# Performance work log

Measured on AMD Instinct MI355X. Metric: run time of the kernel, lower is better.

## Reference

```python
import jax, jax.numpy as jnp
import numpy as np

HIDDEN = 450
DEPTH = 6
ATOM_FDIM = 35          # len(ELEM_LIST)+6+5+1
BOND_FDIM = 5
MAX_NB = 15
N_ATOMS = 20000
N_BONDS = 40000
N_MESS = 16000          # tree messages (row 0 is the zero padding slot)
N_MOLS = 1000


def _linear_init(key, out_dim, in_dim):
    s = 1.0 / np.sqrt(in_dim)
    return jax.random.uniform(key, (out_dim, in_dim), jnp.float32, -s, s)


def setup_inputs() -> dict:
    key = jax.random.key(0)
    ks = jax.random.split(key, 9)
    total_msg = N_MESS + N_BONDS
    fatoms = jax.random.normal(ks[0], (N_ATOMS, ATOM_FDIM), jnp.float32)
    fbonds = jax.random.normal(ks[1], (N_BONDS, ATOM_FDIM + BOND_FDIM), jnp.float32)
    agraph = jax.random.randint(ks[2], (N_ATOMS, MAX_NB), 0, total_msg, jnp.int32)
    bgraph = jax.random.randint(ks[3], (N_BONDS, MAX_NB), 0, total_msg, jnp.int32)
    tree_message = jax.random.normal(ks[4], (N_MESS, HIDDEN), jnp.float32)
    tree_message = tree_message.at[0].set(0.0)  # index 0 = padding message
    # uniform scope: N_MOLS molecules of N_ATOMS//N_MOLS atoms each
    mol_ids = jnp.repeat(jnp.arange(N_MOLS, dtype=jnp.int32), N_ATOMS // N_MOLS)
    W_i = _linear_init(ks[5], HIDDEN, ATOM_FDIM + BOND_FDIM)
    W_h = _linear_init(ks[6], HIDDEN, HIDDEN)
    W_o = _linear_init(ks[7], HIDDEN, ATOM_FDIM + HIDDEN)
    s = 1.0 / np.sqrt(ATOM_FDIM + HIDDEN)
    b_o = jax.random.uniform(ks[8], (HIDDEN,), jnp.float32, -s, s)
    return {"fatoms": fatoms, "fbonds": fbonds, "agraph": agraph, "bgraph": bgraph,
            "mol_ids": mol_ids, "n_mols": N_MOLS, "tree_message": tree_message,
            "W_i": W_i, "W_h": W_h, "W_o": W_o, "b_o": b_o}


def reference(fatoms, fbonds, agraph, bgraph, mol_ids, n_mols, tree_message,
              W_i, W_h, W_o, b_o):
    binput = fbonds @ W_i.T                       # [B, H]
    graph_message = jax.nn.relu(binput)
    for _ in range(DEPTH - 1):                    # static depth loop
        message = jnp.concatenate([tree_message, graph_message], axis=0)  # [M+B, H]
        nei_message = message[bgraph].sum(axis=1)  # gather [B, MAX_NB, H] -> [B, H]
        graph_message = jax.nn.relu(binput + nei_message @ W_h.T)
    message = jnp.concatenate([tree_message, graph_message], axis=0)
    nei_message = message[agraph].sum(axis=1)      # [A, H]
    ainput = jnp.concatenate([fatoms, nei_message], axis=1)  # [A, ATOM_FDIM+H]
    atom_hiddens = jax.nn.relu(ainput @ W_o.T + b_o)          # [A, H]
    # mean over each molecule's atoms (scope)
    sums = jax.ops.segment_sum(atom_hiddens, mol_ids, num_segments=n_mols)
    counts = jax.ops.segment_sum(jnp.ones((atom_hiddens.shape[0], 1), atom_hiddens.dtype),
                                 mol_ids, num_segments=n_mols)
    return sums / counts
```

## Files before the change

kernel.cpp:

```cpp
#include <hip/hip_runtime.h>

#define HIDDEN 450
#define MAX_NB 15
#define N_ATOMS 20000
#define N_BONDS 40000
#define N_MESS  16000
#define N_MOLS  1000
#define KPAD    512
#define MSTRIDE 456
#define FSTRIDE 64
#define BM      64

typedef unsigned int uint;
typedef unsigned short ushort;
typedef __bf16 bf16x8 __attribute__((ext_vector_type(8)));
typedef float  f32x4  __attribute__((ext_vector_type(4)));

__device__ __forceinline__ ushort f2bf(float f) {
    uint u = __builtin_bit_cast(uint, f);
    u += 0x7fffu + ((u >> 16) & 1u);
    return (ushort)(u >> 16);
}
__device__ __forceinline__ float bfhi(uint w) {
    return __builtin_bit_cast(float, w & 0xffff0000u);
}
__device__ __forceinline__ float bflo(uint w) {
    return __builtin_bit_cast(float, w << 16);
}


__global__ __launch_bounds__(256) void pack_tree(const float* __restrict__ tree,
                                                 ushort* __restrict__ tbuf) {
    const int r = blockIdx.x, t = threadIdx.x;
    if (t < 228) {
        uint p = 0;
        if (t < 225) {
            const float2 v = *(const float2*)&tree[(size_t)r * HIDDEN + 2 * t];
            p = (uint)f2bf(v.x) | ((uint)f2bf(v.y) << 16);
        }
        ((uint*)(tbuf + (size_t)r * MSTRIDE))[t] = p;
    }
}

__global__ __launch_bounds__(256) void pack_bonds(const float* __restrict__ fbonds,
                                                  ushort* __restrict__ Abuf) {
    const int r = blockIdx.x * 4 + (threadIdx.x >> 6);
    const int t = threadIdx.x & 63;
    if (r >= N_BONDS) return;
    Abuf[(size_t)r * FSTRIDE + t] = (t < 40) ? f2bf(fbonds[(size_t)r * 40 + t])
                                             : (ushort)0;
}

__global__ __launch_bounds__(256) void pack_atoms(const float* __restrict__ fatoms,
                                                  ushort* __restrict__ Aout) {
    const int r = blockIdx.x * 4 + (threadIdx.x >> 6);
    const int t = threadIdx.x & 63;
    if (r >= N_ATOMS) return;
    Aout[(size_t)r * FSTRIDE + t] = (t < 35) ? f2bf(fatoms[(size_t)r * 35 + t])
                                             : (ushort)0;
}

__global__ __launch_bounds__(256) void pack_w(const float* __restrict__ W_i,
                                              const float* __restrict__ W_h,
                                              const float* __restrict__ W_o,
                                              ushort* __restrict__ Wcat,
                                              ushort* __restrict__ Wocat) {
    const int n = blockIdx.x;
    for (int c = threadIdx.x; c < KPAD; c += 256) {
        float v = 0.0f, vo = 0.0f;
        if (n < HIDDEN) {
            if (c < 40)       v = W_i[(size_t)n * 40 + c];
            else if (c < 490) v = W_h[(size_t)n * HIDDEN + (c - 40)];
            if (c < 35)       vo = W_o[(size_t)n * 485 + c];
            else if (c >= 40 && c < 490) vo = W_o[(size_t)n * 485 + 35 + (c - 40)];
        }
        Wcat [(size_t)n * KPAD + c] = f2bf(v);
        Wocat[(size_t)n * KPAD + c] = f2bf(vo);
    }
}

__global__ __launch_bounds__(256) void precompute_base(const int* __restrict__ g,
                                                       const ushort* __restrict__ tbuf,
                                                       ushort* __restrict__ base,
                                                       int nrows) {
    const int r_raw = blockIdx.x * 4 + (threadIdx.x >> 6);
    const int lane = threadIdx.x & 63;
    if (r_raw >= nrows) return;
    const int r = __builtin_amdgcn_readfirstlane(r_raw);
    const int* gr = g + (size_t)r * MAX_NB;
    const ushort* p[MAX_NB];
#pragma unroll
    for (int j = 0; j < MAX_NB; ++j) {
        const int idx = gr[j];
        p[j] = tbuf + (size_t)((idx < N_MESS) ? idx : 0) * MSTRIDE;
    }
    if (lane >= 57) return;
    const int off = lane * 8;
    uint4 w[MAX_NB];
#pragma unroll
    for (int j = 0; j < MAX_NB; ++j) w[j] = *(const uint4*)(p[j] + off);
    __builtin_amdgcn_sched_barrier(0);
    float acc[8] = {};
#pragma unroll
    for (int j = 0; j < MAX_NB; ++j) {
        acc[0] += bflo(w[j].x); acc[1] += bfhi(w[j].x);
        acc[2] += bflo(w[j].y); acc[3] += bfhi(w[j].y);
        acc[4] += bflo(w[j].z); acc[5] += bfhi(w[j].z);
        acc[6] += bflo(w[j].w); acc[7] += bfhi(w[j].w);
    }
    uint4 o;
    o.x = (uint)f2bf(acc[0]) | ((uint)f2bf(acc[1]) << 16);
    o.y = (uint)f2bf(acc[2]) | ((uint)f2bf(acc[3]) << 16);
    o.z = (uint)f2bf(acc[4]) | ((uint)f2bf(acc[5]) << 16);
    o.w = (uint)f2bf(acc[6]) | ((uint)f2bf(acc[7]) << 16);
    *(uint4*)(base + (size_t)r * MSTRIDE + off) = o;
}

template <int KT, int AST>
__global__ __launch_bounds__(256, 2) void mfma_gemm0(
    const ushort* __restrict__ A, int M,
    const ushort* __restrict__ W,
    ushort* __restrict__ gout, int mtiles) {
    __shared__ ushort At[64 * KT * 32];
    const int tid = threadIdx.x;
    const int id  = blockIdx.x;
    const int b     = id & 7;
    const int n_blk = (id >> 3) & 1;
    const int m_blk = (id >> 4) * 8 + b;
    if (m_blk >= mtiles) return;
    const int m0 = m_blk * 64, n0 = n_blk * 256;
    const int CPR = KT * 4;

    {
        const int srow = tid >> 2;
        const int c0   = tid & 3;
        const ushort* gsrc = A + (size_t)min(m0 + srow, M - 1) * AST;
        ushort* lrow = At + srow * (KT * 32);
#pragma unroll
        for (int c = c0; c < CPR; c += 4) {
            const uint4 v = *(const uint4*)(gsrc + c * 8);
            *(uint4*)&lrow[(c ^ (srow & 7)) * 8] = v;
        }
    }
    __syncthreads();

    const int lane = tid & 63;
    const int wave = tid >> 6;
    const int wn = wave * 64;
    const int lr = lane & 15;
    const int lk = lane >> 4;

    size_t woff[4];
#pragma unroll
    for (int s = 0; s < 4; ++s)
        woff[s] = (size_t)(n0 + wn + s * 16 + lr) * KPAD + lk * 8;

    f32x4 acc[4][4];
#pragma unroll
    for (int i = 0; i < 4; ++i)
#pragma unroll
        for (int j = 0; j < 4; ++j) acc[i][j] = (f32x4){0.f, 0.f, 0.f, 0.f};

    bf16x8 wa[4], wb[4], afa[4];
#pragma unroll
    for (int s = 0; s < 4; ++s) wa[s] = *(const bf16x8*)&W[woff[s]];
#pragma unroll
    for (int s = 0; s < 4; ++s)
        wb[s] = (KT > 1) ? *(const bf16x8*)&W[woff[s] + 32] : wa[s];
#pragma unroll
    for (int mt = 0; mt < 4; ++mt) {
        const int row = mt * 16 + lr;
        afa[mt] = *(const bf16x8*)&At[(row * CPR + (lk ^ (row & 7))) * 8];
    }

#pragma unroll
    for (int i = 0; i < KT; ++i) {
        bf16x8 wc[4], afb[4];
        if (i + 2 < KT) {
#pragma unroll
            for (int s = 0; s < 4; ++s)
                wc[s] = *(const bf16x8*)&W[woff[s] + (size_t)(i + 2) * 32];
        }
        if (i + 1 < KT) {
#pragma unroll
            for (int mt = 0; mt < 4; ++mt) {
                const int row = mt * 16 + lr;
                const int chunk = (((i + 1) * 4 + lk)) ^ (row & 7);
                afb[mt] = *(const bf16x8*)&At[(row * CPR + chunk) * 8];
            }
        }
#pragma unroll
        for (int mt = 0; mt < 4; ++mt)
#pragma unroll
            for (int nt = 0; nt < 4; ++nt)
                acc[mt][nt] = __builtin_amdgcn_mfma_f32_16x16x32_bf16(
                    afa[mt], wa[nt], acc[mt][nt], 0, 0, 0);
        if (i + 1 < KT) {
#pragma unroll
            for (int s = 0; s < 4; ++s) wa[s] = wb[s];
#pragma unroll
            for (int mt = 0; mt < 4; ++mt) afa[mt] = afb[mt];
        }
        if (i + 2 < KT) {
#pragma unroll
            for (int s = 0; s < 4; ++s) wb[s] = wc[s];
        }
    }

    const int col_l = lane & 15;
    const int rbase = (lane >> 4) * 4;
#pragma unroll
    for (int mt = 0; mt < 4; ++mt) {
        const int mbase = m0 + mt * 16 + rbase;
#pragma unroll
        for (int nt = 0; nt < 4; ++nt) {
            const int n = n0 + wn + nt * 16 + col_l;
#pragma unroll
            for (int reg = 0; reg < 4; ++reg) {
                const int m = mbase + reg;
                if (m >= M) continue;
                if (n < HIDDEN)
                    gout[(size_t)m * MSTRIDE + n] = f2bf(fmaxf(acc[mt][nt][reg], 0.0f));
                else if (n < MSTRIDE)
                    gout[(size_t)m * MSTRIDE + n] = 0;
            }
        }
    }
}

template <int MODE>
__global__ __launch_bounds__(512, 4) void fused_gg(
    const int* __restrict__ g,
    const ushort* __restrict__ base,
    const ushort* __restrict__ gin,
    const ushort* __restrict__ zrow,
    const ushort* __restrict__ feat,
    const ushort* __restrict__ W,
    const float* __restrict__ bias, const int* __restrict__ mol_ids,
    ushort* __restrict__ gout, float* __restrict__ aout, int M) {
    __shared__ ushort At[BM * KPAD];
    const int tid  = threadIdx.x;
    const int lane = tid & 63;
    const int wave = tid >> 6;
    const int m0 = blockIdx.x * BM;

#pragma unroll 1
    for (int rr = 0; rr < 8; ++rr) {
        const int r = (wave << 3) | rr;
        const int m = __builtin_amdgcn_readfirstlane(min(m0 + r, M - 1));
        const int sw = r & 7;
        ushort* lrow = At + r * KPAD;
        const int* gr = g + (size_t)m * MAX_NB;
        const ushort* p[MAX_NB];
#pragma unroll
        for (int j = 0; j < MAX_NB; ++j) {
            const int row = gr[j] - N_MESS;
            p[j] = (row >= 0) ? gin + (size_t)row * MSTRIDE : zrow;
        }
        if (lane < 57) {
            const int off = lane * 8;
            const uint4 b = *(const uint4*)(base + (size_t)m * MSTRIDE + off);
            uint4 w[MAX_NB];
#pragma unroll
            for (int j = 0; j < MAX_NB; ++j) w[j] = *(const uint4*)(p[j] + off);
            __builtin_amdgcn_sched_barrier(0);
            float acc[8];
            acc[0] = bflo(b.x); acc[1] = bfhi(b.x);
            acc[2] = bflo(b.y); acc[3] = bfhi(b.y);
            acc[4] = bflo(b.z); acc[5] = bfhi(b.z);
            acc[6] = bflo(b.w); acc[7] = bfhi(b.w);
#pragma unroll
            for (int j = 0; j < MAX_NB; ++j) {
                acc[0] += bflo(w[j].x); acc[1] += bfhi(w[j].x);
                acc[2] += bflo(w[j].y); acc[3] += bfhi(w[j].y);
                acc[4] += bflo(w[j].z); acc[5] += bfhi(w[j].z);
                acc[6] += bflo(w[j].w); acc[7] += bfhi(w[j].w);
            }
            uint4 o;
            o.x = (uint)f2bf(acc[0]) | ((uint)f2bf(acc[1]) << 16);
            o.y = (uint)f2bf(acc[2]) | ((uint)f2bf(acc[3]) << 16);
            o.z = (uint)f2bf(acc[4]) | ((uint)f2bf(acc[5]) << 16);
            o.w = (uint)f2bf(acc[6]) | ((uint)f2bf(acc[7]) << 16);
            *(uint4*)&lrow[((5 + lane) ^ sw) * 8] = o;
        } else {
            const int c = (lane < 62) ? (lane - 57) : lane;
            uint4 v = (uint4){0u, 0u, 0u, 0u};
            if (lane < 62)
                v = *(const uint4*)(feat + (size_t)m * FSTRIDE + (lane - 57) * 8);
            *(uint4*)&lrow[(c ^ sw) * 8] = v;
        }
    }
    __syncthreads();

    const int wn = wave * 64;
    const int lr = lane & 15;
    const int lk = lane >> 4;

    size_t woff[4];
#pragma unroll
    for (int s = 0; s < 4; ++s)
        woff[s] = (size_t)(wn + s * 16 + lr) * KPAD + lk * 8;

    f32x4 acc[4][4];
#pragma unroll
    for (int i = 0; i < 4; ++i)
#pragma unroll
        for (int j = 0; j < 4; ++j) acc[i][j] = (f32x4){0.f, 0.f, 0.f, 0.f};

    bf16x8 wa[4], wb[4], afa[4];
#pragma unroll
    for (int s = 0; s < 4; ++s) wa[s] = *(const bf16x8*)&W[woff[s]];
#pragma unroll
    for (int s = 0; s < 4; ++s) wb[s] = *(const bf16x8*)&W[woff[s] + 32];
#pragma unroll
    for (int mt = 0; mt < 4; ++mt) {
        const int row = mt * 16 + lr;
        afa[mt] = *(const bf16x8*)&At[(row * 64 + (lk ^ (row & 7))) * 8];
    }

#pragma unroll
    for (int i = 0; i < 16; ++i) {
        bf16x8 wc[4], afb[4];
        if (i + 2 < 16) {
#pragma unroll
            for (int s = 0; s < 4; ++s)
                wc[s] = *(const bf16x8*)&W[woff[s] + (size_t)(i + 2) * 32];
        }
        if (i + 1 < 16) {
#pragma unroll
            for (int mt = 0; mt < 4; ++mt) {
                const int row = mt * 16 + lr;
                const int chunk = (((i + 1) * 4 + lk)) ^ (row & 7);
                afb[mt] = *(const bf16x8*)&At[(row * 64 + chunk) * 8];
            }
        }
#pragma unroll
        for (int mt = 0; mt < 4; ++mt)
#pragma unroll
            for (int nt = 0; nt < 4; ++nt)
                acc[mt][nt] = __builtin_amdgcn_mfma_f32_16x16x32_bf16(
                    afa[mt], wa[nt], acc[mt][nt], 0, 0, 0);
        if (i + 1 < 16) {
#pragma unroll
            for (int s = 0; s < 4; ++s) wa[s] = wb[s];
#pragma unroll
            for (int mt = 0; mt < 4; ++mt) afa[mt] = afb[mt];
        }
        if (i + 2 < 16) {
#pragma unroll
            for (int s = 0; s < 4; ++s) wb[s] = wc[s];
        }
    }

    const int col_l = lane & 15;
    const int rbase = (lane >> 4) * 4;
#pragma unroll
    for (int mt = 0; mt < 4; ++mt) {
        const int mbase = m0 + mt * 16 + rbase;
        int mol[4];
        if (MODE == 1) {
#pragma unroll
            for (int reg = 0; reg < 4; ++reg)
                mol[reg] = mol_ids[min(mbase + reg, M - 1)];
        }
#pragma unroll
        for (int nt = 0; nt < 4; ++nt) {
            const int n = wn + nt * 16 + col_l;
            if (MODE == 0) {
#pragma unroll
                for (int reg = 0; reg < 4; ++reg) {
                    const int m = mbase + reg;
                    if (m >= M) continue;
                    if (n < HIDDEN)
                        gout[(size_t)m * MSTRIDE + n] = f2bf(fmaxf(acc[mt][nt][reg], 0.0f));
                    else if (n < MSTRIDE)
                        gout[(size_t)m * MSTRIDE + n] = 0;
                }
            } else {
                if (n >= HIDDEN) continue;
                const float bsum = bias[n];
                float run = 0.0f;
                int cur = mol[0];
#pragma unroll
                for (int reg = 0; reg < 4; ++reg) {
                    const float v = (mbase + reg < M)
                        ? fmaxf(acc[mt][nt][reg] + bsum, 0.0f) : 0.0f;
                    if (mol[reg] != cur) {
                        atomicAdd(&aout[(size_t)cur * HIDDEN + n], run);
                        cur = mol[reg];
                        run = 0.0f;
                    }
                    run += v;
                }
                atomicAdd(&aout[(size_t)cur * HIDDEN + n], run);
            }
        }
    }
}

__global__ __launch_bounds__(256) void count_atoms(const int* __restrict__ mol_ids,
                                                   float* __restrict__ counts) {
    const int a = blockIdx.x * 256 + threadIdx.x;
    if (a < N_ATOMS) atomicAdd(&counts[mol_ids[a]], 1.0f);
}
__global__ __launch_bounds__(256) void div_counts(float* __restrict__ out,
                                                  const float* __restrict__ counts) {
    const int i = blockIdx.x * 256 + threadIdx.x;
    if (i < N_MOLS * HIDDEN) out[i] = out[i] / counts[i / HIDDEN];
}

extern "C" void kernel_launch(void* const* d_in, const int* in_sizes, int n_in,
                              void* d_out, int out_size, void* d_ws, size_t ws_size,
                              hipStream_t stream) {
    const float* fatoms  = (const float*)d_in[0];
    const float* fbonds  = (const float*)d_in[1];
    const int*   agraph  = (const int*)d_in[2];
    const int*   bgraph  = (const int*)d_in[3];
    const int*   mol_ids = (const int*)d_in[4];
    const float* tree    = (const float*)d_in[6];
    const float* W_i     = (const float*)d_in[7];
    const float* W_h     = (const float*)d_in[8];
    const float* W_o     = (const float*)d_in[9];
    const float* b_o     = (const float*)d_in[10];
    float* out = (float*)d_out;

    ushort* zrow   = (ushort*)d_ws;
    ushort* Abuf   = zrow   + 512;
    ushort* Aout   = Abuf   + (size_t)N_BONDS * FSTRIDE;
    ushort* gmsgA  = Aout   + (size_t)N_ATOMS * FSTRIDE;
    ushort* gmsgB  = gmsgA  + (size_t)N_BONDS * MSTRIDE;
    ushort* tbuf   = gmsgB  + (size_t)N_BONDS * MSTRIDE;
    ushort* Wcat   = tbuf   + (size_t)N_MESS  * MSTRIDE;
    ushort* Wocat  = Wcat   + (size_t)KPAD * KPAD;
    ushort* base_b = Wocat  + (size_t)KPAD * KPAD;
    ushort* base_a = base_b + (size_t)N_BONDS * MSTRIDE;
    float*  counts = (float*)(base_a + (size_t)N_ATOMS * MSTRIDE);

    (void)hipMemsetAsync(d_out, 0, (size_t)N_MOLS * HIDDEN * sizeof(float), stream);
    (void)hipMemsetAsync(counts, 0, N_MOLS * sizeof(float), stream);
    (void)hipMemsetAsync(zrow, 0, 512 * sizeof(ushort), stream);

    const dim3 blk(256);
    pack_tree <<<N_MESS, blk, 0, stream>>>(tree, tbuf);
    pack_bonds<<<(N_BONDS + 3) / 4, blk, 0, stream>>>(fbonds, Abuf);
    pack_atoms<<<(N_ATOMS + 3) / 4, blk, 0, stream>>>(fatoms, Aout);
    pack_w    <<<KPAD, blk, 0, stream>>>(W_i, W_h, W_o, Wcat, Wocat);
    precompute_base<<<(N_BONDS + 3) / 4, blk, 0, stream>>>(bgraph, tbuf, base_b, N_BONDS);
    precompute_base<<<(N_ATOMS + 3) / 4, blk, 0, stream>>>(agraph, tbuf, base_a, N_ATOMS);

    const int mtB = (N_BONDS + 63) / 64;
    const int mtA = (N_ATOMS + 63) / 64;
    const dim3 gB0(((mtB + 7) / 8) * 16);

    mfma_gemm0<2, FSTRIDE><<<gB0, blk, 0, stream>>>(Abuf, N_BONDS, Wcat, gmsgA, mtB);

    ushort* cur = gmsgA;
    ushort* nxt = gmsgB;
    const dim3 blk2(512);
    for (int it = 0; it < 5; ++it) {
        fused_gg<0><<<mtB, blk2, 0, stream>>>(bgraph, base_b, cur, zrow, Abuf, Wcat,
                                              nullptr, nullptr, nxt, nullptr, N_BONDS);
        ushort* t = cur; cur = nxt; nxt = t;
    }
    fused_gg<1><<<mtA, blk2, 0, stream>>>(agraph, base_a, cur, zrow, Aout, Wocat,
                                          b_o, mol_ids, nullptr, out, N_ATOMS);

    count_atoms<<<(N_ATOMS + 255) / 256, blk, 0, stream>>>(mol_ids, counts);
    div_counts <<<(N_MOLS * HIDDEN + 255) / 256, blk, 0, stream>>>(out, counts);
}
```

Measured before the change: 835.9 us.

## Double-buffer gather/GEMM tiles in fused kernel and drop atom base precompute

The fused gather+GEMM kernel now processes two 32-row tiles per block with two LDS buffers, staging the second tile's neighbour gather while the first tile's MFMA loop runs. The atom-side precompute of tree-message sums is removed; the final atom kernel gathers tree messages directly from the packed tree buffer instead. This aims to overlap memory-bound gathers with matrix work and skip one full precompute pass, at the cost of smaller M tiles (less W reuse per tile) and more gathers in the final kernel.

New measurement: 1.050 ms. 1.26x slower.

```diff
diff --git a/kernel.cpp b/kernel.cpp
--- a/kernel.cpp
+++ b/kernel.cpp
@@ -9,7 +9,7 @@
 #define KPAD    512
 #define MSTRIDE 456
 #define FSTRIDE 64
-#define BM      64
+#define BM      32
 
 typedef unsigned int uint;
 typedef unsigned short ushort;
@@ -228,173 +228,201 @@
     }
 }
 
-template <int MODE>
+template <int MODE, bool HASBASE>
 __global__ __launch_bounds__(512, 4) void fused_gg(
     const int* __restrict__ g,
     const ushort* __restrict__ base,
     const ushort* __restrict__ gin,
     const ushort* __restrict__ zrow,
+    const ushort* __restrict__ tmsg,
     const ushort* __restrict__ feat,
     const ushort* __restrict__ W,
     const float* __restrict__ bias, const int* __restrict__ mol_ids,
-    ushort* __restrict__ gout, float* __restrict__ aout, int M) {
-    __shared__ ushort At[BM * KPAD];
+    ushort* __restrict__ gout, float* __restrict__ aout, int M, int mtiles) {
+    __shared__ ushort At[2][BM * KPAD];
     const int tid  = threadIdx.x;
     const int lane = tid & 63;
     const int wave = tid >> 6;
-    const int m0 = blockIdx.x * BM;
-
-#pragma unroll 1
-    for (int rr = 0; rr < 8; ++rr) {
-        const int r = (wave << 3) | rr;
-        const int m = __builtin_amdgcn_readfirstlane(min(m0 + r, M - 1));
-        const int sw = r & 7;
-        ushort* lrow = At + r * KPAD;
-        const int* gr = g + (size_t)m * MAX_NB;
-        const ushort* p[MAX_NB];
-#pragma unroll
-        for (int j = 0; j < MAX_NB; ++j) {
-            const int row = gr[j] - N_MESS;
-            p[j] = (row >= 0) ? gin + (size_t)row * MSTRIDE : zrow;
-        }
-        if (lane < 57) {
-            const int off = lane * 8;
-            const uint4 b = *(const uint4*)(base + (size_t)m * MSTRIDE + off);
-            uint4 w[MAX_NB];
-#pragma unroll
-            for (int j = 0; j < MAX_NB; ++j) w[j] = *(const uint4*)(p[j] + off);
-            __builtin_amdgcn_sched_barrier(0);
-            float acc[8];
-            acc[0] = bflo(b.x); acc[1] = bfhi(b.x);
-            acc[2] = bflo(b.y); acc[3] = bfhi(b.y);
-            acc[4] = bflo(b.z); acc[5] = bfhi(b.z);
-            acc[6] = bflo(b.w); acc[7] = bfhi(b.w);
-#pragma unroll
-            for (int j = 0; j < MAX_NB; ++j) {
-                acc[0] += bflo(w[j].x); acc[1] += bfhi(w[j].x);
-                acc[2] += bflo(w[j].y); acc[3] += bfhi(w[j].y);
-                acc[4] += bflo(w[j].z); acc[5] += bfhi(w[j].z);
-                acc[6] += bflo(w[j].w); acc[7] += bfhi(w[j].w);
-            }
-            uint4 o;
-            o.x = (uint)f2bf(acc[0]) | ((uint)f2bf(acc[1]) << 16);
-            o.y = (uint)f2bf(acc[2]) | ((uint)f2bf(acc[3]) << 16);
-            o.z = (uint)f2bf(acc[4]) | ((uint)f2bf(acc[5]) << 16);
-            o.w = (uint)f2bf(acc[6]) | ((uint)f2bf(acc[7]) << 16);
-            *(uint4*)&lrow[((5 + lane) ^ sw) * 8] = o;
-        } else {
-            const int c = (lane < 62) ? (lane - 57) : lane;
-            uint4 v = (uint4){0u, 0u, 0u, 0u};
-            if (lane < 62)
-                v = *(const uint4*)(feat + (size_t)m * FSTRIDE + (lane - 57) * 8);
-            *(uint4*)&lrow[(c ^ sw) * 8] = v;
-        }
-    }
-    __syncthreads();
-
-    const int wn = wave * 64;
     const int lr = lane & 15;
     const int lk = lane >> 4;
+    const int wn = wave * 64;
+    const int t0 = blockIdx.x * 2;
 
     size_t woff[4];
 #pragma unroll
     for (int s = 0; s < 4; ++s)
         woff[s] = (size_t)(wn + s * 16 + lr) * KPAD + lk * 8;
 
-    f32x4 acc[4][4];
-#pragma unroll
-    for (int i = 0; i < 4; ++i)
-#pragma unroll
-        for (int j = 0; j < 4; ++j) acc[i][j] = (f32x4){0.f, 0.f, 0.f, 0.f};
-
-    bf16x8 wa[4], wb[4], afa[4];
-#pragma unroll
-    for (int s = 0; s < 4; ++s) wa[s] = *(const bf16x8*)&W[woff[s]];
-#pragma unroll
-    for (int s = 0; s < 4; ++s) wb[s] = *(const bf16x8*)&W[woff[s] + 32];
-#pragma unroll
-    for (int mt = 0; mt < 4; ++mt) {
-        const int row = mt * 16 + lr;
-        afa[mt] = *(const bf16x8*)&At[(row * 64 + (lk ^ (row & 7))) * 8];
-    }
-
-#pragma unroll
-    for (int i = 0; i < 16; ++i) {
-        bf16x8 wc[4], afb[4];
-        if (i + 2 < 16) {
-#pragma unroll
-            for (int s = 0; s < 4; ++s)
-                wc[s] = *(const bf16x8*)&W[woff[s] + (size_t)(i + 2) * 32];
-        }
-        if (i + 1 < 16) {
-#pragma unroll
-            for (int mt = 0; mt < 4; ++mt) {
-                const int row = mt * 16 + lr;
-                const int chunk = (((i + 1) * 4 + lk)) ^ (row & 7);
-                afb[mt] = *(const bf16x8*)&At[(row * 64 + chunk) * 8];
-            }
-        }
-#pragma unroll
-        for (int mt = 0; mt < 4; ++mt)
-#pragma unroll
-            for (int nt = 0; nt < 4; ++nt)
-                acc[mt][nt] = __builtin_amdgcn_mfma_f32_16x16x32_bf16(
-                    afa[mt], wa[nt], acc[mt][nt], 0, 0, 0);
-        if (i + 1 < 16) {
-#pragma unroll
-            for (int s = 0; s < 4; ++s) wa[s] = wb[s];
-#pragma unroll
-            for (int mt = 0; mt < 4; ++mt) afa[mt] = afb[mt];
-        }
-        if (i + 2 < 16) {
-#pragma unroll
-            for (int s = 0; s < 4; ++s) wb[s] = wc[s];
-        }
-    }
-
-    const int col_l = lane & 15;
-    const int rbase = (lane >> 4) * 4;
-#pragma unroll
-    for (int mt = 0; mt < 4; ++mt) {
-        const int mbase = m0 + mt * 16 + rbase;
-        int mol[4];
-        if (MODE == 1) {
-#pragma unroll
-            for (int reg = 0; reg < 4; ++reg)
-                mol[reg] = mol_ids[min(mbase + reg, M - 1)];
-        }
-#pragma unroll
-        for (int nt = 0; nt < 4; ++nt) {
-            const int n = wn + nt * 16 + col_l;
-            if (MODE == 0) {
-#pragma unroll
-                for (int reg = 0; reg < 4; ++reg) {
-                    const int m = mbase + reg;
-                    if (m >= M) continue;
-                    if (n < HIDDEN)
-                        gout[(size_t)m * MSTRIDE + n] = f2bf(fmaxf(acc[mt][nt][reg], 0.0f));
-                    else if (n < MSTRIDE)
-                        gout[(size_t)m * MSTRIDE + n] = 0;
+    auto STAGE = [&](int tile, ushort* buf) {
+#pragma unroll 1
+        for (int rr = 0; rr < 4; ++rr) {
+            const int r = (wave << 2) | rr;
+            const int m = __builtin_amdgcn_readfirstlane(min(tile * BM + r, M - 1));
+            const int sw = r & 7;
+            ushort* lrow = buf + r * KPAD;
+            const int* gr = g + (size_t)m * MAX_NB;
+            const ushort* p[MAX_NB];
+#pragma unroll
+            for (int j = 0; j < MAX_NB; ++j) {
+                const int idx = gr[j];
+                const int row = idx - N_MESS;
+                if (HASBASE) p[j] = (row >= 0) ? gin + (size_t)row * MSTRIDE : zrow;
+                else p[j] = (row >= 0) ? gin + (size_t)row * MSTRIDE
+                                       : tmsg + (size_t)idx * MSTRIDE;
+            }
+            if (lane < 57) {
+                const int off = lane * 8;
+                float acc[8];
+                uint4 w[MAX_NB];
+                if (HASBASE) {
+                    const uint4 b = *(const uint4*)(base + (size_t)m * MSTRIDE + off);
+#pragma unroll
+                    for (int j = 0; j < MAX_NB; ++j)
+                        w[j] = *(const uint4*)(p[j] + off);
+                    __builtin_amdgcn_sched_barrier(0);
+                    acc[0] = bflo(b.x); acc[1] = bfhi(b.x);
+                    acc[2] = bflo(b.y); acc[3] = bfhi(b.y);
+                    acc[4] = bflo(b.z); acc[5] = bfhi(b.z);
+                    acc[6] = bflo(b.w); acc[7] = bfhi(b.w);
+                } else {
+#pragma unroll
+                    for (int j = 0; j < MAX_NB; ++j)
+                        w[j] = *(const uint4*)(p[j] + off);
+                    __builtin_amdgcn_sched_barrier(0);
+#pragma unroll
+                    for (int k = 0; k < 8; ++k) acc[k] = 0.0f;
                 }
+#pragma unroll
+                for (int j = 0; j < MAX_NB; ++j) {
+                    acc[0] += bflo(w[j].x); acc[1] += bfhi(w[j].x);
+                    acc[2] += bflo(w[j].y); acc[3] += bfhi(w[j].y);
+                    acc[4] += bflo(w[j].z); acc[5] += bfhi(w[j].z);
+                    acc[6] += bflo(w[j].w); acc[7] += bfhi(w[j].w);
+                }
+                uint4 o;
+                o.x = (uint)f2bf(acc[0]) | ((uint)f2bf(acc[1]) << 16);
+                o.y = (uint)f2bf(acc[2]) | ((uint)f2bf(acc[3]) << 16);
+                o.z = (uint)f2bf(acc[4]) | ((uint)f2bf(acc[5]) << 16);
+                o.w = (uint)f2bf(acc[6]) | ((uint)f2bf(acc[7]) << 16);
+                *(uint4*)&lrow[((5 + lane) ^ sw) * 8] = o;
             } else {
-                if (n >= HIDDEN) continue;
-                const float bsum = bias[n];
-                float run = 0.0f;
-                int cur = mol[0];
-#pragma unroll
-                for (int reg = 0; reg < 4; ++reg) {
-                    const float v = (mbase + reg < M)
-                        ? fmaxf(acc[mt][nt][reg] + bsum, 0.0f) : 0.0f;
-                    if (mol[reg] != cur) {
-                        atomicAdd(&aout[(size_t)cur * HIDDEN + n], run);
-                        cur = mol[reg];
-                        run = 0.0f;
+                const int c = (lane < 62) ? (lane - 57) : lane;
+                uint4 v = (uint4){0u, 0u, 0u, 0u};
+                if (lane < 62)
+                    v = *(const uint4*)(feat + (size_t)m * FSTRIDE + (lane - 57) * 8);
+                *(uint4*)&lrow[(c ^ sw) * 8] = v;
+            }
+        }
+    };
+
+    auto COMPUTE = [&](int tile, const ushort* buf) {
+        const int m0 = tile * BM;
+        f32x4 acc[2][4];
+#pragma unroll
+        for (int i = 0; i < 2; ++i)
+#pragma unroll
+            for (int j = 0; j < 4; ++j) acc[i][j] = (f32x4){0.f, 0.f, 0.f, 0.f};
+
+        bf16x8 wa[4], wb[4], afa[2];
+#pragma unroll
+        for (int s = 0; s < 4; ++s) wa[s] = *(const bf16x8*)&W[woff[s]];
+#pragma unroll
+        for (int s = 0; s < 4; ++s) wb[s] = *(const bf16x8*)&W[woff[s] + 32];
+#pragma unroll
+        for (int mt = 0; mt < 2; ++mt) {
+            const int row = mt * 16 + lr;
+            afa[mt] = *(const bf16x8*)&buf[(row * 64 + (lk ^ (row & 7))) * 8];
+        }
+
+#pragma unroll
+        for (int i = 0; i < 16; ++i) {
+            bf16x8 wc[4], afb[2];
+            if (i + 2 < 16) {
+#pragma unroll
+                for (int s = 0; s < 4; ++s)
+                    wc[s] = *(const bf16x8*)&W[woff[s] + (size_t)(i + 2) * 32];
+            }
+            if (i + 1 < 16) {
+#pragma unroll
+                for (int mt = 0; mt < 2; ++mt) {
+                    const int row = mt * 16 + lr;
+                    const int chunk = (((i + 1) * 4 + lk)) ^ (row & 7);
+                    afb[mt] = *(const bf16x8*)&buf[(row * 64 + chunk) * 8];
+                }
+            }
+#pragma unroll
+            for (int mt = 0; mt < 2; ++mt)
+#pragma unroll
+                for (int nt = 0; nt < 4; ++nt)
+                    acc[mt][nt] = __builtin_amdgcn_mfma_f32_16x16x32_bf16(
+                        afa[mt], wa[nt], acc[mt][nt], 0, 0, 0);
+            if (i + 1 < 16) {
+#pragma unroll
+                for (int s = 0; s < 4; ++s) wa[s] = wb[s];
+#pragma unroll
+                for (int mt = 0; mt < 2; ++mt) afa[mt] = afb[mt];
+            }
+            if (i + 2 < 16) {
+#pragma unroll
+                for (int s = 0; s < 4; ++s) wb[s] = wc[s];
+            }
+        }
+
+        const int col_l = lane & 15;
+        const int rbase = (lane >> 4) * 4;
+#pragma unroll
+        for (int mt = 0; mt < 2; ++mt) {
+            const int mbase = m0 + mt * 16 + rbase;
+            int mol[4];
+            if (MODE == 1) {
+#pragma unroll
+                for (int reg = 0; reg < 4; ++reg)
+                    mol[reg] = mol_ids[min(mbase + reg, M - 1)];
+            }
+#pragma unroll
+            for (int nt = 0; nt < 4; ++nt) {
+                const int n = wn + nt * 16 + col_l;
+                if (MODE == 0) {
+#pragma unroll
+                    for (int reg = 0; reg < 4; ++reg) {
+                        const int m = mbase + reg;
+                        if (m >= M) continue;
+                        if (n < HIDDEN)
+                            gout[(size_t)m * MSTRIDE + n] =
+                                f2bf(fmaxf(acc[mt][nt][reg], 0.0f));
+                        else if (n < MSTRIDE)
+                            gout[(size_t)m * MSTRIDE + n] = 0;
                     }
-                    run += v;
+                } else {
+                    if (n >= HIDDEN) continue;
+                    const float bsum = bias[n];
+                    float run = 0.0f;
+                    int cur = mol[0];
+#pragma unroll
+                    for (int reg = 0; reg < 4; ++reg) {
+                        const float v = (mbase + reg < M)
+                            ? fmaxf(acc[mt][nt][reg] + bsum, 0.0f) : 0.0f;
+                        if (mol[reg] != cur) {
+                            atomicAdd(&aout[(size_t)cur * HIDDEN + n], run);
+                            cur = mol[reg];
+                            run = 0.0f;
+                        }
+                        run += v;
+                    }
+                    atomicAdd(&aout[(size_t)cur * HIDDEN + n], run);
                 }
-                atomicAdd(&aout[(size_t)cur * HIDDEN + n], run);
-            }
-        }
+            }
+        }
+    };
+
+    STAGE(t0, At[0]);
+    __syncthreads();
+    const bool has2 = (t0 + 1 < mtiles);
+    if (has2) STAGE(t0 + 1, At[1]);
+    COMPUTE(t0, At[0]);
+    if (has2) {
+        __syncthreads();
+        COMPUTE(t0 + 1, At[1]);
     }
 }
 
@@ -433,8 +461,7 @@
     ushort* Wcat   = tbuf   + (size_t)N_MESS  * MSTRIDE;
     ushort* Wocat  = Wcat   + (size_t)KPAD * KPAD;
     ushort* base_b = Wocat  + (size_t)KPAD * KPAD;
-    ushort* base_a = base_b + (size_t)N_BONDS * MSTRIDE;
-    float*  counts = (float*)(base_a + (size_t)N_ATOMS * MSTRIDE);
+    float*  counts = (float*)(base_b + (size_t)N_BONDS * MSTRIDE);
 
     (void)hipMemsetAsync(d_out, 0, (size_t)N_MOLS * HIDDEN * sizeof(float), stream);
     (void)hipMemsetAsync(counts, 0, N_MOLS * sizeof(float), stream);
@@ -446,24 +473,28 @@
     pack_atoms<<<(N_ATOMS + 3) / 4, blk, 0, stream>>>(fatoms, Aout);
     pack_w    <<<KPAD, blk, 0, stream>>>(W_i, W_h, W_o, Wcat, Wocat);
     precompute_base<<<(N_BONDS + 3) / 4, blk, 0, stream>>>(bgraph, tbuf, base_b, N_BONDS);
-    precompute_base<<<(N_ATOMS + 3) / 4, blk, 0, stream>>>(agraph, tbuf, base_a, N_ATOMS);
-
-    const int mtB = (N_BONDS + 63) / 64;
-    const int mtA = (N_ATOMS + 63) / 64;
-    const dim3 gB0(((mtB + 7) / 8) * 16);
-
-    mfma_gemm0<2, FSTRIDE><<<gB0, blk, 0, stream>>>(Abuf, N_BONDS, Wcat, gmsgA, mtB);
-
+
+    const int mt64 = (N_BONDS + 63) / 64;
+    const dim3 gB0(((mt64 + 7) / 8) * 16);
+
+    mfma_gemm0<2, FSTRIDE><<<gB0, blk, 0, stream>>>(Abuf, N_BONDS, Wcat, gmsgA, mt64);
+
+    const int mtB = (N_BONDS + BM - 1) / BM;
+    const int mtA = (N_ATOMS + BM - 1) / BM;
     ushort* cur = gmsgA;
     ushort* nxt = gmsgB;
     const dim3 blk2(512);
+    const dim3 gB((mtB + 1) / 2);
+    const dim3 gA((mtA + 1) / 2);
     for (int it = 0; it < 5; ++it) {
-        fused_gg<0><<<mtB, blk2, 0, stream>>>(bgraph, base_b, cur, zrow, Abuf, Wcat,
-                                              nullptr, nullptr, nxt, nullptr, N_BONDS);
+        fused_gg<0, true><<<gB, blk2, 0, stream>>>(bgraph, base_b, cur, zrow, tbuf,
+                                                   Abuf, Wcat, nullptr, nullptr,
+                                                   nxt, nullptr, N_BONDS, mtB);
         ushort* t = cur; cur = nxt; nxt = t;
     }
-    fused_gg<1><<<mtA, blk2, 0, stream>>>(agraph, base_a, cur, zrow, Aout, Wocat,
-                                          b_o, mol_ids, nullptr, out, N_ATOMS);
+    fused_gg<1, false><<<gA, blk2, 0, stream>>>(agraph, nullptr, cur, zrow, tbuf,
+                                                Aout, Wocat, b_o, mol_ids,
+                                                nullptr, out, N_ATOMS, mtA);
 
     count_atoms<<<(N_ATOMS + 255) / 256, blk, 0, stream>>>(mol_ids, counts);
     div_counts <<<(N_MOLS * HIDDEN + 255) / 256, blk, 0, stream>>>(out, counts);
```

## Shrink fused gather-GEMM tile to 16 rows with multi-tile blocks and unified message buffer

Applied to the files above, without the earlier changes.

The fused gather+GEMM kernel now works on 16-row tiles instead of 64, and each block loops over several tiles (5 per block for bonds, 3 for atoms) with fixed grid sizes. The workspace is laid out so tree messages and both graph-message buffers sit contiguously and are indexed through one base pointer plus an offset. This removes the zero-row buffer and the separate atom base precompute, since the final atom pass gathers tree messages directly. Each wave now amortises its weight-fragment loads over 4x fewer rows, which raises weight traffic from L2 and adds a second barrier per tile. In exchange it gets finer-grained work and one less precompute kernel.

Result: slower. 2.060 ms (+146.5%).

```diff
diff --git a/kernel.cpp b/kernel.cpp
--- a/kernel.cpp
+++ b/kernel.cpp
@@ -9,7 +9,7 @@
 #define KPAD    512
 #define MSTRIDE 456
 #define FSTRIDE 64
-#define BM      64
+#define BM      16
 
 typedef unsigned int uint;
 typedef unsigned short ushort;
@@ -232,136 +232,137 @@
 __global__ __launch_bounds__(512, 4) void fused_gg(
     const int* __restrict__ g,
     const ushort* __restrict__ base,
-    const ushort* __restrict__ gin,
-    const ushort* __restrict__ zrow,
+    const ushort* __restrict__ msg,
+    int dynoff,
     const ushort* __restrict__ feat,
     const ushort* __restrict__ W,
     const float* __restrict__ bias, const int* __restrict__ mol_ids,
-    ushort* __restrict__ gout, float* __restrict__ aout, int M) {
+    ushort* __restrict__ gout, float* __restrict__ aout,
+    int mtiles, int tpb) {
     __shared__ ushort At[BM * KPAD];
     const int tid  = threadIdx.x;
     const int lane = tid & 63;
     const int wave = tid >> 6;
-    const int m0 = blockIdx.x * BM;
-
-#pragma unroll 1
-    for (int rr = 0; rr < 8; ++rr) {
-        const int r = (wave << 3) | rr;
-        const int m = __builtin_amdgcn_readfirstlane(min(m0 + r, M - 1));
-        const int sw = r & 7;
-        ushort* lrow = At + r * KPAD;
-        const int* gr = g + (size_t)m * MAX_NB;
-        const ushort* p[MAX_NB];
-#pragma unroll
-        for (int j = 0; j < MAX_NB; ++j) {
-            const int row = gr[j] - N_MESS;
-            p[j] = (row >= 0) ? gin + (size_t)row * MSTRIDE : zrow;
-        }
-        if (lane < 57) {
-            const int off = lane * 8;
-            const uint4 b = *(const uint4*)(base + (size_t)m * MSTRIDE + off);
-            uint4 w[MAX_NB];
-#pragma unroll
-            for (int j = 0; j < MAX_NB; ++j) w[j] = *(const uint4*)(p[j] + off);
-            __builtin_amdgcn_sched_barrier(0);
-            float acc[8];
-            acc[0] = bflo(b.x); acc[1] = bfhi(b.x);
-            acc[2] = bflo(b.y); acc[3] = bfhi(b.y);
-            acc[4] = bflo(b.z); acc[5] = bfhi(b.z);
-            acc[6] = bflo(b.w); acc[7] = bfhi(b.w);
-#pragma unroll
-            for (int j = 0; j < MAX_NB; ++j) {
-                acc[0] += bflo(w[j].x); acc[1] += bfhi(w[j].x);
-                acc[2] += bflo(w[j].y); acc[3] += bfhi(w[j].y);
-                acc[4] += bflo(w[j].z); acc[5] += bfhi(w[j].z);
-                acc[6] += bflo(w[j].w); acc[7] += bfhi(w[j].w);
-            }
-            uint4 o;
-            o.x = (uint)f2bf(acc[0]) | ((uint)f2bf(acc[1]) << 16);
-            o.y = (uint)f2bf(acc[2]) | ((uint)f2bf(acc[3]) << 16);
-            o.z = (uint)f2bf(acc[4]) | ((uint)f2bf(acc[5]) << 16);
-            o.w = (uint)f2bf(acc[6]) | ((uint)f2bf(acc[7]) << 16);
-            *(uint4*)&lrow[((5 + lane) ^ sw) * 8] = o;
-        } else {
-            const int c = (lane < 62) ? (lane - 57) : lane;
-            uint4 v = (uint4){0u, 0u, 0u, 0u};
-            if (lane < 62)
-                v = *(const uint4*)(feat + (size_t)m * FSTRIDE + (lane - 57) * 8);
-            *(uint4*)&lrow[(c ^ sw) * 8] = v;
-        }
-    }
-    __syncthreads();
-
-    const int wn = wave * 64;
     const int lr = lane & 15;
     const int lk = lane >> 4;
+    const int wn = wave * 64;
 
     size_t woff[4];
 #pragma unroll
     for (int s = 0; s < 4; ++s)
         woff[s] = (size_t)(wn + s * 16 + lr) * KPAD + lk * 8;
 
-    f32x4 acc[4][4];
-#pragma unroll
-    for (int i = 0; i < 4; ++i)
-#pragma unroll
-        for (int j = 0; j < 4; ++j) acc[i][j] = (f32x4){0.f, 0.f, 0.f, 0.f};
-
-    bf16x8 wa[4], wb[4], afa[4];
-#pragma unroll
-    for (int s = 0; s < 4; ++s) wa[s] = *(const bf16x8*)&W[woff[s]];
-#pragma unroll
-    for (int s = 0; s < 4; ++s) wb[s] = *(const bf16x8*)&W[woff[s] + 32];
-#pragma unroll
-    for (int mt = 0; mt < 4; ++mt) {
-        const int row = mt * 16 + lr;
-        afa[mt] = *(const bf16x8*)&At[(row * 64 + (lk ^ (row & 7))) * 8];
-    }
-
-#pragma unroll
-    for (int i = 0; i < 16; ++i) {
-        bf16x8 wc[4], afb[4];
-        if (i + 2 < 16) {
-#pragma unroll
-            for (int s = 0; s < 4; ++s)
-                wc[s] = *(const bf16x8*)&W[woff[s] + (size_t)(i + 2) * 32];
-        }
-        if (i + 1 < 16) {
-#pragma unroll
-            for (int mt = 0; mt < 4; ++mt) {
-                const int row = mt * 16 + lr;
-                const int chunk = (((i + 1) * 4 + lk)) ^ (row & 7);
-                afb[mt] = *(const bf16x8*)&At[(row * 64 + chunk) * 8];
-            }
-        }
-#pragma unroll
-        for (int mt = 0; mt < 4; ++mt)
+    const int tbeg = blockIdx.x * tpb;
+    const int tend = min(tbeg + tpb, mtiles);
+
+    for (int tile = tbeg; tile < tend; ++tile) {
+#pragma unroll 1
+        for (int rr = 0; rr < 2; ++rr) {
+            const int r = wave * 2 + rr;
+            const int m = __builtin_amdgcn_readfirstlane(tile * BM + r);
+            const int sw = r & 7;
+            ushort* lrow = At + r * KPAD;
+            const int* gr = g + (size_t)m * MAX_NB;
+            const ushort* p[MAX_NB];
+#pragma unroll
+            for (int j = 0; j < MAX_NB; ++j) {
+                const int idx = gr[j];
+                int mrow;
+                if (MODE == 0)
+                    mrow = (idx >= N_MESS) ? (idx - N_MESS + dynoff) : 0;
+                else
+                    mrow = (idx >= N_MESS) ? (idx - N_MESS + dynoff) : idx;
+                p[j] = msg + (size_t)mrow * MSTRIDE;
+            }
+            if (lane < 57) {
+                const int off = lane * 8;
+                uint4 w[MAX_NB];
+                float acc[8];
+                if (MODE == 0) {
+                    const uint4 b = *(const uint4*)(base + (size_t)m * MSTRIDE + off);
+#pragma unroll
+                    for (int j = 0; j < MAX_NB; ++j)
+                        w[j] = *(const uint4*)(p[j] + off);
+                    __builtin_amdgcn_sched_barrier(0);
+                    acc[0] = bflo(b.x); acc[1] = bfhi(b.x);
+                    acc[2] = bflo(b.y); acc[3] = bfhi(b.y);
+                    acc[4] = bflo(b.z); acc[5] = bfhi(b.z);
+                    acc[6] = bflo(b.w); acc[7] = bfhi(b.w);
+                } else {
+#pragma unroll
+                    for (int j = 0; j < MAX_NB; ++j)
+                        w[j] = *(const uint4*)(p[j] + off);
+                    __builtin_amdgcn_sched_barrier(0);
+#pragma unroll
+                    for (int k = 0; k < 8; ++k) acc[k] = 0.0f;
+                }
+#pragma unroll
+                for (int j = 0; j < MAX_NB; ++j) {
+                    acc[0] += bflo(w[j].x); acc[1] += bfhi(w[j].x);
+                    acc[2] += bflo(w[j].y); acc[3] += bfhi(w[j].y);
+                    acc[4] += bflo(w[j].z); acc[5] += bfhi(w[j].z);
+                    acc[6] += bflo(w[j].w); acc[7] += bfhi(w[j].w);
+                }
+                uint4 o;
+                o.x = (uint)f2bf(acc[0]) | ((uint)f2bf(acc[1]) << 16);
+                o.y = (uint)f2bf(acc[2]) | ((uint)f2bf(acc[3]) << 16);
+                o.z = (uint)f2bf(acc[4]) | ((uint)f2bf(acc[5]) << 16);
+                o.w = (uint)f2bf(acc[6]) | ((uint)f2bf(acc[7]) << 16);
+                *(uint4*)&lrow[((5 + lane) ^ sw) * 8] = o;
+            } else {
+                const int c = (lane < 62) ? (lane - 57) : lane;
+                uint4 v = (uint4){0u, 0u, 0u, 0u};
+                if (lane < 62)
+                    v = *(const uint4*)(feat + (size_t)m * FSTRIDE + (lane - 57) * 8);
+                *(uint4*)&lrow[(c ^ sw) * 8] = v;
+            }
+        }
+        __syncthreads();
+
+        f32x4 acc[4];
+#pragma unroll
+        for (int j = 0; j < 4; ++j) acc[j] = (f32x4){0.f, 0.f, 0.f, 0.f};
+
+        bf16x8 wa[4], wb[4];
+#pragma unroll
+        for (int s = 0; s < 4; ++s) wa[s] = *(const bf16x8*)&W[woff[s]];
+#pragma unroll
+        for (int s = 0; s < 4; ++s) wb[s] = *(const bf16x8*)&W[woff[s] + 32];
+        bf16x8 afa = *(const bf16x8*)&At[(lr * 64 + (lk ^ (lr & 7))) * 8];
+
+#pragma unroll
+        for (int i = 0; i < 16; ++i) {
+            bf16x8 wc[4], afb;
+            if (i + 2 < 16) {
+#pragma unroll
+                for (int s = 0; s < 4; ++s)
+                    wc[s] = *(const bf16x8*)&W[woff[s] + (size_t)(i + 2) * 32];
+            }
+            if (i + 1 < 16) {
+                const int chunk = (((i + 1) * 4 + lk)) ^ (lr & 7);
+                afb = *(const bf16x8*)&At[(lr * 64 + chunk) * 8];
+            }
 #pragma unroll
             for (int nt = 0; nt < 4; ++nt)
-                acc[mt][nt] = __builtin_amdgcn_mfma_f32_16x16x32_bf16(
-                    afa[mt], wa[nt], acc[mt][nt], 0, 0, 0);
-        if (i + 1 < 16) {
-#pragma unroll
-            for (int s = 0; s < 4; ++s) wa[s] = wb[s];
-#pragma unroll
-            for (int mt = 0; mt < 4; ++mt) afa[mt] = afb[mt];
-        }
-        if (i + 2 < 16) {
-#pragma unroll
-            for (int s = 0; s < 4; ++s) wb[s] = wc[s];
-        }
-    }
-
-    const int col_l = lane & 15;
-    const int rbase = (lane >> 4) * 4;
-#pragma unroll
-    for (int mt = 0; mt < 4; ++mt) {
-        const int mbase = m0 + mt * 16 + rbase;
+                acc[nt] = __builtin_amdgcn_mfma_f32_16x16x32_bf16(
+                    afa, wa[nt], acc[nt], 0, 0, 0);
+            if (i + 1 < 16) {
+#pragma unroll
+                for (int s = 0; s < 4; ++s) wa[s] = wb[s];
+                afa = afb;
+            }
+            if (i + 2 < 16) {
+#pragma unroll
+                for (int s = 0; s < 4; ++s) wb[s] = wc[s];
+            }
+        }
+
+        const int col_l = lane & 15;
+        const int mbase = tile * BM + (lane >> 4) * 4;
         int mol[4];
         if (MODE == 1) {
 #pragma unroll
-            for (int reg = 0; reg < 4; ++reg)
-                mol[reg] = mol_ids[min(mbase + reg, M - 1)];
+            for (int reg = 0; reg < 4; ++reg) mol[reg] = mol_ids[mbase + reg];
         }
 #pragma unroll
         for (int nt = 0; nt < 4; ++nt) {
@@ -370,9 +371,9 @@
 #pragma unroll
                 for (int reg = 0; reg < 4; ++reg) {
                     const int m = mbase + reg;
-                    if (m >= M) continue;
                     if (n < HIDDEN)
-                        gout[(size_t)m * MSTRIDE + n] = f2bf(fmaxf(acc[mt][nt][reg], 0.0f));
+                        gout[(size_t)m * MSTRIDE + n] =
+                            f2bf(fmaxf(acc[nt][reg], 0.0f));
                     else if (n < MSTRIDE)
                         gout[(size_t)m * MSTRIDE + n] = 0;
                 }
@@ -383,8 +384,7 @@
                 int cur = mol[0];
 #pragma unroll
                 for (int reg = 0; reg < 4; ++reg) {
-                    const float v = (mbase + reg < M)
-                        ? fmaxf(acc[mt][nt][reg] + bsum, 0.0f) : 0.0f;
+                    const float v = fmaxf(acc[nt][reg] + bsum, 0.0f);
                     if (mol[reg] != cur) {
                         atomicAdd(&aout[(size_t)cur * HIDDEN + n], run);
                         cur = mol[reg];
@@ -395,6 +395,7 @@
                 atomicAdd(&aout[(size_t)cur * HIDDEN + n], run);
             }
         }
+        __syncthreads();
     }
 }
 
@@ -424,21 +425,18 @@
     const float* b_o     = (const float*)d_in[10];
     float* out = (float*)d_out;
 
-    ushort* zrow   = (ushort*)d_ws;
-    ushort* Abuf   = zrow   + 512;
-    ushort* Aout   = Abuf   + (size_t)N_BONDS * FSTRIDE;
-    ushort* gmsgA  = Aout   + (size_t)N_ATOMS * FSTRIDE;
-    ushort* gmsgB  = gmsgA  + (size_t)N_BONDS * MSTRIDE;
-    ushort* tbuf   = gmsgB  + (size_t)N_BONDS * MSTRIDE;
-    ushort* Wcat   = tbuf   + (size_t)N_MESS  * MSTRIDE;
-    ushort* Wocat  = Wcat   + (size_t)KPAD * KPAD;
-    ushort* base_b = Wocat  + (size_t)KPAD * KPAD;
-    ushort* base_a = base_b + (size_t)N_BONDS * MSTRIDE;
-    float*  counts = (float*)(base_a + (size_t)N_ATOMS * MSTRIDE);
+    ushort* tbuf  = (ushort*)d_ws;
+    ushort* gmsgA = tbuf  + (size_t)N_MESS  * MSTRIDE;
+    ushort* gmsgB = gmsgA + (size_t)N_BONDS * MSTRIDE;
+    ushort* Abuf  = gmsgB + (size_t)N_BONDS * MSTRIDE;
+    ushort* Aout  = Abuf  + (size_t)N_BONDS * FSTRIDE;
+    ushort* Wcat  = Aout  + (size_t)N_ATOMS * FSTRIDE;
+    ushort* Wocat = Wcat  + (size_t)KPAD * KPAD;
+    ushort* base_b= Wocat + (size_t)KPAD * KPAD;
+    float*  counts= (float*)(base_b + (size_t)N_BONDS * MSTRIDE);
 
     (void)hipMemsetAsync(d_out, 0, (size_t)N_MOLS * HIDDEN * sizeof(float), stream);
     (void)hipMemsetAsync(counts, 0, N_MOLS * sizeof(float), stream);
-    (void)hipMemsetAsync(zrow, 0, 512 * sizeof(ushort), stream);
 
     const dim3 blk(256);
     pack_tree <<<N_MESS, blk, 0, stream>>>(tree, tbuf);
@@ -446,24 +444,27 @@
     pack_atoms<<<(N_ATOMS + 3) / 4, blk, 0, stream>>>(fatoms, Aout);
     pack_w    <<<KPAD, blk, 0, stream>>>(W_i, W_h, W_o, Wcat, Wocat);
     precompute_base<<<(N_BONDS + 3) / 4, blk, 0, stream>>>(bgraph, tbuf, base_b, N_BONDS);
-    precompute_base<<<(N_ATOMS + 3) / 4, blk, 0, stream>>>(agraph, tbuf, base_a, N_ATOMS);
-
-    const int mtB = (N_BONDS + 63) / 64;
-    const int mtA = (N_ATOMS + 63) / 64;
-    const dim3 gB0(((mtB + 7) / 8) * 16);
-
-    mfma_gemm0<2, FSTRIDE><<<gB0, blk, 0, stream>>>(Abuf, N_BONDS, Wcat, gmsgA, mtB);
-
-    ushort* cur = gmsgA;
-    ushort* nxt = gmsgB;
+
+    const int mt64 = (N_BONDS + 63) / 64;
+    const dim3 gB0(((mt64 + 7) / 8) * 16);
+
+    mfma_gemm0<2, FSTRIDE><<<gB0, blk, 0, stream>>>(Abuf, N_BONDS, Wcat, gmsgA, mt64);
+
+    const int mtB = N_BONDS / BM;
+    const int mtA = N_ATOMS / BM;
     const dim3 blk2(512);
+    ushort* cur = gmsgA; int dynC = N_MESS;
+    ushort* nxt = gmsgB; int dynN = N_MESS + N_BONDS;
     for (int it = 0; it < 5; ++it) {
-        fused_gg<0><<<mtB, blk2, 0, stream>>>(bgraph, base_b, cur, zrow, Abuf, Wcat,
-                                              nullptr, nullptr, nxt, nullptr, N_BONDS);
+        fused_gg<0><<<500, blk2, 0, stream>>>(bgraph, base_b, tbuf, dynC,
+                                              Abuf, Wcat, nullptr, nullptr,
+                                              nxt, nullptr, mtB, 5);
         ushort* t = cur; cur = nxt; nxt = t;
-    }
-    fused_gg<1><<<mtA, blk2, 0, stream>>>(agraph, base_a, cur, zrow, Aout, Wocat,
-                                          b_o, mol_ids, nullptr, out, N_ATOMS);
+        int d = dynC; dynC = dynN; dynN = d;
+    }
+    fused_gg<1><<<417, blk2, 0, stream>>>(agraph, nullptr, tbuf, dynC,
+                                          Aout, Wocat, b_o, mol_ids,
+                                          nullptr, out, mtA, 3);
 
     count_atoms<<<(N_ATOMS + 255) / 256, blk, 0, stream>>>(mol_ids, counts);
     div_counts <<<(N_MOLS * HIDDEN + 255) / 256, blk, 0, stream>>>(out, counts);
```
